# Kernel tuning notes

Hardware: AMD Instinct MI355X
Metric: run time of the kernel (lower is better)

## Reference

```python
import jax, jax.numpy as jnp
import numpy as np

N = 100_000          # nodes
E = 1_600_000        # edges (avg degree 16)
NODE_SCA, NODE_VEC = 4, 3
EDGE_SCA, EDGE_VEC = 6, 3
OUT_SCA, OUT_VEC = 16, 16
CUTOFF = 10.0
EPS = 1e-6
SLOPE_VN = 0.2       # VNLeakyReLU negative slope (SurfGen default)
SLOPE_SCA = 0.01     # nn.LeakyReLU default


def setup_inputs() -> dict:
    key = jax.random.key(0)
    ks = jax.random.split(key, 22)
    rn = lambda k, s: jax.random.normal(k, s, dtype=jnp.float32)
    return {
        # forward args
        'node_sca': rn(ks[0], (N, NODE_SCA)),
        'node_vec': rn(ks[1], (N, NODE_VEC, 3)),
        'edge_sca': rn(ks[2], (E, EDGE_SCA)),
        'edge_vec': rn(ks[3], (E, EDGE_VEC, 3)),
        'gds_dist': jax.random.uniform(ks[4], (E,), dtype=jnp.float32) * 12.0,
        'edge_index': jax.random.randint(ks[5], (2, E), 0, N),
        # message projections (Linear weights stored [in,out])
        'W_nss': rn(ks[6], (NODE_SCA, OUT_SCA)) * 0.3, 'b_nss': rn(ks[7], (OUT_SCA,)) * 0.1,
        'W_ess': rn(ks[8], (EDGE_SCA, OUT_SCA)) * 0.3, 'b_ess': rn(ks[9], (OUT_SCA,)) * 0.1,
        'W_nsv': rn(ks[10], (NODE_SCA, OUT_SCA)) * 0.3, 'b_nsv': rn(ks[11], (OUT_SCA,)) * 0.1,
        'W_esv': rn(ks[12], (EDGE_SCA, OUT_SCA)) * 0.3, 'b_esv': rn(ks[13], (OUT_SCA,)) * 0.1,
        'W_nvv': rn(ks[14], (NODE_VEC, OUT_VEC)) * 0.3,   # VNLinear (no bias)
        'W_evv': rn(ks[15], (EDGE_VEC, OUT_VEC)) * 0.3,
        # GVPerceptronVN(16,16,16,16): GVLinear (dim_hid = 16) + VN LeakyReLU
        'W_lv':  rn(ks[16], (OUT_VEC, OUT_VEC)) * 0.25,   # lin_vector   (no bias)
        'W_lv2': rn(ks[17], (OUT_VEC, OUT_VEC)) * 0.25,   # lin_vector2  (no bias)
        'W_ls':  rn(ks[18], (OUT_VEC + OUT_SCA, OUT_SCA)) * 0.25,  # lin_scalar (no bias)
        'W_gate': rn(ks[19], (OUT_SCA, OUT_VEC)) * 0.25, 'b_gate': rn(ks[20], (OUT_VEC,)) * 0.1,
        'W_dir': rn(ks[21], (OUT_VEC, OUT_VEC)) * 0.25,   # VNLeakyReLU direction (no bias)
    }


def vn_linear(x, W):
    # x: [n, c_in, 3], W: [c_in, c_out] -> [n, c_out, 3]
    return jnp.einsum('nci,co->noi', x, W)


def reference(node_sca, node_vec, edge_sca, edge_vec, gds_dist, edge_index,
              W_nss, b_nss, W_ess, b_ess, W_nsv, b_nsv, W_esv, b_esv,
              W_nvv, W_evv, W_lv, W_lv2, W_ls, W_gate, b_gate, W_dir):
    src = edge_index[0]
    num_nodes = node_sca.shape[0]

    # cosine cutoff coefficient
    coeff = 0.5 * (jnp.cos(gds_dist * (jnp.pi / CUTOFF)) + 1.0)
    coeff = coeff * (gds_dist <= CUTOFF) * (gds_dist >= 0.0)  # [E]

    # scalar message: gather node proj, mix with edge proj, cutoff-weight
    node_ss = node_sca @ W_nss + b_nss                          # [N,16]
    edge_ss = edge_sca @ W_ess + b_ess                          # [E,16]
    msg_sca = node_ss[src] * edge_ss * coeff[:, None]           # [E,16]

    # vector message
    node_vv = vn_linear(node_vec, W_nvv)                        # [N,16,3]
    edge_vv = vn_linear(edge_vec, W_evv)                        # [E,16,3]
    node_sv = node_sca @ W_nsv + b_nsv                          # [N,16]
    edge_sv = edge_sca @ W_esv + b_esv                          # [E,16]
    msg_vec = (node_vv[src] * edge_sv[:, :, None]
               + node_sv[src][:, :, None] * edge_vv) * coeff[:, None, None]  # [E,16,3]

    # scatter_sum into source nodes (matches original's edge_index[0])
    aggr_sca = jax.ops.segment_sum(msg_sca, src, num_segments=num_nodes)  # [N,16]
    aggr_vec = jax.ops.segment_sum(msg_vec, src, num_segments=num_nodes)  # [N,16,3]

    # --- GVPerceptronVN: GVLinear ---
    v_inter = vn_linear(aggr_vec, W_lv)                          # [N,16,3]
    v_norm = jnp.sqrt(jnp.sum(v_inter * v_inter, axis=-1))       # [N,16]
    out_sca = jnp.concatenate([v_norm, aggr_sca], axis=-1) @ W_ls  # [N,16]
    out_vec = vn_linear(v_inter, W_lv2)                          # [N,16,3]
    gate = jax.nn.sigmoid(out_sca @ W_gate + b_gate)[:, :, None]
    out_vec = gate * out_vec

    # --- VNLeakyReLU on vectors ---
    d = vn_linear(out_vec, W_dir)                                # [N,16,3]
    dot = jnp.sum(out_vec * d, axis=-1, keepdims=True)
    mask = (dot >= 0).astype(out_vec.dtype)
    d_norm_sq = jnp.sum(d * d, axis=-1, keepdims=True)
    out_vec = SLOPE_VN * out_vec + (1.0 - SLOPE_VN) * (
        mask * out_vec + (1.0 - mask) * (out_vec - (dot / (d_norm_sq + EPS)) * d))

    # LeakyReLU on scalars
    out_sca = jnp.where(out_sca >= 0, out_sca, SLOPE_SCA * out_sca)
    return out_sca, out_vec
```

## Files before the change

### kernel.cpp

```cpp
#include <hip/hip_runtime.h>
#include <hip/hip_fp16.h>
#include <math.h>

#define CUTOFF_F 10.0f
#define PI_OVER_CUTOFF 0.31415926535897931f
#define KCAP 64
#define KCAP3 32

__global__ __launch_bounds__(256) void bucket_scatter(
    const float* __restrict__ edge_sca,
    const float* __restrict__ edge_vec,
    const float* __restrict__ gds,
    const int* __restrict__ eidx,
    int* __restrict__ count,
    __half* __restrict__ bucket,
    float* __restrict__ aggr,
    int E)
{
    int e = blockIdx.x * blockDim.x + threadIdx.x;
    if (e >= E) return;

    int src = eidx[e];
    float d = gds[e];
    float c = 0.0f;
    if (d >= 0.0f && d <= CUTOFF_F)
        c = 0.5f * (__cosf(d * PI_OVER_CUTOFF) + 1.0f);

    const float* es = edge_sca + (size_t)e * 6;
    const float* ev = edge_vec + (size_t)e * 9;

    float f[16];
#pragma unroll
    for (int i = 0; i < 6; ++i) f[i] = c * es[i];
    f[6] = c;
#pragma unroll
    for (int i = 0; i < 9; ++i) f[7 + i] = c * ev[i];

    int slot = atomicAdd(&count[src], 1);
    if (slot < KCAP3) {
        union { __half h[16]; uint4 u[2]; } pk;
#pragma unroll
        for (int i = 0; i < 16; ++i) pk.h[i] = __float2half(f[i]);
        uint4* pb = (uint4*)(bucket + ((size_t)src * KCAP3 + slot) * 16);
        pb[0] = pk.u[0];
        pb[1] = pk.u[1];
    } else {
        float* base = aggr + (size_t)src * 16;
#pragma unroll
        for (int i = 0; i < 16; ++i) atomicAdd(base + i, f[i]);
    }
}

__global__ __launch_bounds__(256) void count_edges(
    const int* __restrict__ eidx, int* __restrict__ count,
    int* __restrict__ slotOf, int E)
{
    int e = blockIdx.x * blockDim.x + threadIdx.x;
    if (e >= E) return;
    int src = eidx[e];
    slotOf[e] = atomicAdd(&count[src], 1);
}

__global__ __launch_bounds__(256) void scan_block_sums(
    const int* __restrict__ count, int* __restrict__ blockSums, int N)
{
    __shared__ int sdata[256];
    int t = threadIdx.x;
    int i = blockIdx.x * 256 + t;
    sdata[t] = (i < N) ? count[i] : 0;
    __syncthreads();
    for (int off = 128; off > 0; off >>= 1) {
        if (t < off) sdata[t] += sdata[t + off];
        __syncthreads();
    }
    if (t == 0) blockSums[blockIdx.x] = sdata[0];
}

__global__ __launch_bounds__(1024) void scan_exclusive_small(
    int* __restrict__ blockSums, int M)
{
    __shared__ int s[1024];
    int t = threadIdx.x;
    int orig = (t < M) ? blockSums[t] : 0;
    s[t] = orig;
    __syncthreads();
    for (int off = 1; off < 1024; off <<= 1) {
        int v = (t >= off) ? s[t - off] : 0;
        __syncthreads();
        s[t] += v;
        __syncthreads();
    }
    if (t < M) blockSums[t] = s[t] - orig;
}

__global__ __launch_bounds__(256) void scan_final(
    const int* __restrict__ count, const int* __restrict__ blockSums,
    int* __restrict__ offsets, int N)
{
    __shared__ int s[256];
    int t = threadIdx.x;
    int i = blockIdx.x * 256 + t;
    int orig = (i < N) ? count[i] : 0;
    s[t] = orig;
    __syncthreads();
    for (int off = 1; off < 256; off <<= 1) {
        int v = (t >= off) ? s[t - off] : 0;
        __syncthreads();
        s[t] += v;
        __syncthreads();
    }
    if (i < N) offsets[i] = s[t] - orig + blockSums[blockIdx.x];
}

__global__ __launch_bounds__(256) void scatter_payload(
    const float* __restrict__ edge_sca, const float* __restrict__ edge_vec,
    const float* __restrict__ gds, const int* __restrict__ eidx,
    const int* __restrict__ slotOf, const int* __restrict__ offsets,
    __half* __restrict__ payload, int E)
{
    int e = blockIdx.x * blockDim.x + threadIdx.x;
    if (e >= E) return;
    int src = eidx[e];
    float d = gds[e];
    float c = 0.0f;
    if (d >= 0.0f && d <= CUTOFF_F)
        c = 0.5f * (__cosf(d * PI_OVER_CUTOFF) + 1.0f);
    const float* es = edge_sca + (size_t)e * 6;
    const float* ev = edge_vec + (size_t)e * 9;
    union { __half h[16]; uint4 u[2]; } pk;
#pragma unroll
    for (int i = 0; i < 6; ++i) pk.h[i] = __float2half(c * es[i]);
    pk.h[6] = __float2half(c);
#pragma unroll
    for (int i = 0; i < 9; ++i) pk.h[7 + i] = __float2half(c * ev[i]);
    uint4* pb = (uint4*)(payload + (size_t)(offsets[src] + slotOf[e]) * 16);
    pb[0] = pk.u[0];
    pb[1] = pk.u[1];
}

__global__ __launch_bounds__(256) void fill_buckets(
    const int* __restrict__ eidx, int* __restrict__ count,
    int* __restrict__ bucket, int E)
{
    int e = blockIdx.x * blockDim.x + threadIdx.x;
    if (e >= E) return;
    int src = eidx[e];
    int slot = atomicAdd(&count[src], 1);
    if (slot < KCAP) bucket[src * KCAP + slot] = e;
}

__global__ __launch_bounds__(256) void edge_aggregate(
    const float* __restrict__ edge_sca, const float* __restrict__ edge_vec,
    const float* __restrict__ gds, const int* __restrict__ eidx,
    float* __restrict__ aggr, int E)
{
    int e = blockIdx.x * blockDim.x + threadIdx.x;
    if (e >= E) return;
    int src = eidx[e];
    float d = gds[e];
    float coeff = 0.0f;
    if (d >= 0.0f && d <= CUTOFF_F)
        coeff = 0.5f * (__cosf(d * PI_OVER_CUTOFF) + 1.0f);
    float* base = aggr + (size_t)src * 16;
    const float* es = edge_sca + (size_t)e * 6;
    const float* ev = edge_vec + (size_t)e * 9;
#pragma unroll
    for (int c = 0; c < 6; ++c) atomicAdd(base + c, coeff * es[c]);
    atomicAdd(base + 6, coeff);
#pragma unroll
    for (int k = 0; k < 9; ++k) atomicAdd(base + 7 + k, coeff * ev[k]);
}

__global__ __launch_bounds__(256) void node_fused(
    const float* __restrict__ node_sca,
    const float* __restrict__ node_vec,
    const float* __restrict__ edge_sca,
    const float* __restrict__ edge_vec,
    const float* __restrict__ gds,
    const int* __restrict__ count,
    const int* __restrict__ bucket,
    const int* __restrict__ offsets,
    const __half* __restrict__ payload,
    const float* __restrict__ aggr,
    const float* __restrict__ W_nss, const float* __restrict__ b_nss,
    const float* __restrict__ W_ess, const float* __restrict__ b_ess,
    const float* __restrict__ W_nsv, const float* __restrict__ b_nsv,
    const float* __restrict__ W_esv, const float* __restrict__ b_esv,
    const float* __restrict__ W_nvv, const float* __restrict__ W_evv,
    const float* __restrict__ W_lv,  const float* __restrict__ W_lv2,
    const float* __restrict__ W_ls,
    const float* __restrict__ W_gate, const float* __restrict__ b_gate,
    const float* __restrict__ W_dir,
    float* __restrict__ out,
    int N, int mode)
{
    __shared__ float sW_nss[64],  sb_nss[16];
    __shared__ float sW_ess[96],  sb_ess[16];
    __shared__ float sW_nsv[64],  sb_nsv[16];
    __shared__ float sW_esv[96],  sb_esv[16];
    __shared__ float sW_nvv[48],  sW_evv[48];
    __shared__ float sW_lv[256],  sW_lv2[256];
    __shared__ float sW_ls[512];
    __shared__ float sW_gate[256], sb_gate[16];
    __shared__ float sW_dir[256];

    __shared__ float s_in  [16 * 33];
    __shared__ float s_avec[16 * 49];
    __shared__ float s_cat [16 * 33];
    __shared__ float s_vint[16 * 49];
    __shared__ float s_osca[16 * 17];
    __shared__ float s_ovec[16 * 49];

    const int t = threadIdx.x;
    {
        for (int i = t; i < 64;  i += 256) { sW_nss[i] = W_nss[i]; sW_nsv[i] = W_nsv[i]; }
        for (int i = t; i < 96;  i += 256) { sW_ess[i] = W_ess[i]; sW_esv[i] = W_esv[i]; }
        for (int i = t; i < 48;  i += 256) { sW_nvv[i] = W_nvv[i]; sW_evv[i] = W_evv[i]; }
        for (int i = t; i < 256; i += 256) {
            sW_lv[i]   = W_lv[i];
            sW_lv2[i]  = W_lv2[i];
            sW_gate[i] = W_gate[i];
            sW_dir[i]  = W_dir[i];
        }
        for (int i = t; i < 512; i += 256) sW_ls[i] = W_ls[i];
        if (t < 16) {
            sb_nss[t]  = b_nss[t];
            sb_ess[t]  = b_ess[t];
            sb_nsv[t]  = b_nsv[t];
            sb_esv[t]  = b_esv[t];
            sb_gate[t] = b_gate[t];
        }
    }

    const int slot = t >> 4;
    const int o    = t & 15;
    const int n    = blockIdx.x * 16 + slot;
    const bool valid = (n < N);

    if (valid) {
        if (o < 4) s_in[slot * 33 + o]     = node_sca[(size_t)n * 4 + o];
        if (o < 9) s_in[slot * 33 + 4 + o] = node_vec[(size_t)n * 9 + o];
    }

    if (mode == 3) {
        float a0 = 0.f, a1 = 0.f, a2 = 0.f, a3 = 0.f;
        if (valid) {
            int cnt = count[n];
            if (cnt > KCAP3) cnt = KCAP3;
            const __half* p = payload + (size_t)n * KCAP3 * 16 + o;
            int s = 0;
            for (; s + 3 < cnt; s += 4) {
                a0 += __half2float(p[(s + 0) * 16]);
                a1 += __half2float(p[(s + 1) * 16]);
                a2 += __half2float(p[(s + 2) * 16]);
                a3 += __half2float(p[(s + 3) * 16]);
            }
            for (; s < cnt; ++s)
                a0 += __half2float(p[s * 16]);
            a1 += aggr[(size_t)n * 16 + o];
            s_in[slot * 33 + 13 + o] = (a0 + a1) + (a2 + a3);
        }
    } else if (mode == 2) {
        float a0 = 0.f, a1 = 0.f, a2 = 0.f, a3 = 0.f;
        if (valid) {
            int cnt = count[n];
            const __half* p = payload + (size_t)offsets[n] * 16 + o;
            int s = 0;
            for (; s + 3 < cnt; s += 4) {
                a0 += __half2float(p[(size_t)(s + 0) * 16]);
                a1 += __half2float(p[(size_t)(s + 1) * 16]);
                a2 += __half2float(p[(size_t)(s + 2) * 16]);
                a3 += __half2float(p[(size_t)(s + 3) * 16]);
            }
            for (; s < cnt; ++s)
                a0 += __half2float(p[(size_t)s * 16]);
            s_in[slot * 33 + 13 + o] = (a0 + a1) + (a2 + a3);
        }
    } else if (mode == 1) {
        float acc = 0.0f;
        int cnt = valid ? count[n] : 0;
        if (cnt > KCAP) cnt = KCAP;
        const int* bk = bucket + (size_t)n * KCAP;
        for (int s = 0; s < cnt; ++s) {
            int e = bk[s];
            float d = gds[e];
            float coeff = 0.0f;
            if (d >= 0.0f && d <= CUTOFF_F)
                coeff = 0.5f * (__cosf(d * PI_OVER_CUTOFF) + 1.0f);
            float feat;
            if (o < 6)       feat = edge_sca[(size_t)e * 6 + o];
            else if (o == 6) feat = 1.0f;
            else             feat = edge_vec[(size_t)e * 9 + (o - 7)];
            acc += coeff * feat;
        }
        if (valid) s_in[slot * 33 + 13 + o] = acc;
    } else {
        if (valid) s_in[slot * 33 + 13 + o] = aggr[(size_t)n * 16 + o];
    }
    __syncthreads();

    const float* in = s_in + slot * 33;

    float nss = sb_nss[o], nsv = sb_nsv[o];
#pragma unroll
    for (int c = 0; c < 4; ++c) {
        float x = in[c];
        nss += x * sW_nss[c * 16 + o];
        nsv += x * sW_nsv[c * 16 + o];
    }
    float nvv0 = 0.f, nvv1 = 0.f, nvv2 = 0.f;
#pragma unroll
    for (int c = 0; c < 3; ++c) {
        float w = sW_nvv[c * 16 + o];
        nvv0 += in[4 + c * 3 + 0] * w;
        nvv1 += in[4 + c * 3 + 1] * w;
        nvv2 += in[4 + c * 3 + 2] * w;
    }
    float cc = in[19];
    float es = cc * sb_ess[o], ev = cc * sb_esv[o];
#pragma unroll
    for (int c = 0; c < 6; ++c) {
        float a = in[13 + c];
        es += a * sW_ess[c * 16 + o];
        ev += a * sW_esv[c * 16 + o];
    }
    float EV0 = 0.f, EV1 = 0.f, EV2 = 0.f;
#pragma unroll
    for (int c = 0; c < 3; ++c) {
        float w = sW_evv[c * 16 + o];
        EV0 += in[20 + c * 3 + 0] * w;
        EV1 += in[20 + c * 3 + 1] * w;
        EV2 += in[20 + c * 3 + 2] * w;
    }

    float asca = nss * es;
    float av0 = nvv0 * ev + nsv * EV0;
    float av1 = nvv1 * ev + nsv * EV1;
    float av2 = nvv2 * ev + nsv * EV2;
    s_avec[slot * 49 + o * 3 + 0] = av0;
    s_avec[slot * 49 + o * 3 + 1] = av1;
    s_avec[slot * 49 + o * 3 + 2] = av2;
    s_cat[slot * 33 + 16 + o] = asca;
    __syncthreads();

    float vi0 = 0.f, vi1 = 0.f, vi2 = 0.f;
#pragma unroll
    for (int c = 0; c < 16; ++c) {
        float w = sW_lv[c * 16 + o];
        const float* a = &s_avec[slot * 49 + c * 3];
        vi0 += a[0] * w; vi1 += a[1] * w; vi2 += a[2] * w;
    }
    float vnorm = sqrtf(vi0 * vi0 + vi1 * vi1 + vi2 * vi2);
    s_vint[slot * 49 + o * 3 + 0] = vi0;
    s_vint[slot * 49 + o * 3 + 1] = vi1;
    s_vint[slot * 49 + o * 3 + 2] = vi2;
    s_cat[slot * 33 + o] = vnorm;
    __syncthreads();

    float osca = 0.f;
#pragma unroll
    for (int c = 0; c < 32; ++c)
        osca += s_cat[slot * 33 + c] * sW_ls[c * 16 + o];
    float ov0 = 0.f, ov1 = 0.f, ov2 = 0.f;
#pragma unroll
    for (int c = 0; c < 16; ++c) {
        float w = sW_lv2[c * 16 + o];
        const float* a = &s_vint[slot * 49 + c * 3];
        ov0 += a[0] * w; ov1 += a[1] * w; ov2 += a[2] * w;
    }
    s_osca[slot * 17 + o] = osca;
    __syncthreads();

    float g = sb_gate[o];
#pragma unroll
    for (int c = 0; c < 16; ++c)
        g += s_osca[slot * 17 + c] * sW_gate[c * 16 + o];
    g = 1.0f / (1.0f + __expf(-g));
    ov0 *= g; ov1 *= g; ov2 *= g;
    s_ovec[slot * 49 + o * 3 + 0] = ov0;
    s_ovec[slot * 49 + o * 3 + 1] = ov1;
    s_ovec[slot * 49 + o * 3 + 2] = ov2;
    __syncthreads();

    float dv0 = 0.f, dv1 = 0.f, dv2 = 0.f;
#pragma unroll
    for (int c = 0; c < 16; ++c) {
        float w = sW_dir[c * 16 + o];
        const float* a = &s_ovec[slot * 49 + c * 3];
        dv0 += a[0] * w; dv1 += a[1] * w; dv2 += a[2] * w;
    }
    float dot = ov0 * dv0 + ov1 * dv1 + ov2 * dv2;
    if (dot < 0.0f) {
        float dn = dv0 * dv0 + dv1 * dv1 + dv2 * dv2;
        float f = 0.8f * dot / (dn + 1e-6f);
        ov0 -= f * dv0; ov1 -= f * dv1; ov2 -= f * dv2;
    }

    if (valid) {
        float so = (osca >= 0.0f) ? osca : 0.01f * osca;
        out[(size_t)n * 16 + o] = so;
        size_t vb = (size_t)N * 16 + (size_t)n * 48 + (size_t)o * 3;
        out[vb + 0] = ov0;
        out[vb + 1] = ov1;
        out[vb + 2] = ov2;
    }
}

extern "C" void kernel_launch(void* const* d_in, const int* in_sizes, int n_in,
                              void* d_out, int out_size, void* d_ws, size_t ws_size,
                              hipStream_t stream)
{
    const float* node_sca = (const float*)d_in[0];
    const float* node_vec = (const float*)d_in[1];
    const float* edge_sca = (const float*)d_in[2];
    const float* edge_vec = (const float*)d_in[3];
    const float* gds      = (const float*)d_in[4];
    const int*   eidx     = (const int*)d_in[5];

    const int N = in_sizes[0] / 4;
    const int E = in_sizes[4];

    int*    count3  = (int*)d_ws;
    float*  aggr3   = (float*)(count3 + N);
    __half* bucket3 = (__half*)(aggr3 + (size_t)N * 16);
    size_t  need3   = (size_t)N * 4 + (size_t)N * 64
                    + (size_t)N * KCAP3 * 16 * sizeof(__half);

    int*    count     = (int*)d_ws;
    int*    offsets   = count + N;
    int*    blockSums = offsets + N;
    int*    slotOf    = blockSums + 1024;
    size_t  hdr_bytes = ((size_t)(2 * N + 1024 + E) * 4 + 63) & ~(size_t)63;
    __half* payload   = (__half*)((char*)d_ws + hdr_bytes);
    size_t  need_csr  = hdr_bytes + (size_t)E * 16 * sizeof(__half);
    size_t  need_bkt  = (size_t)N * (1 + KCAP) * sizeof(int);

    const int nBlocksN = (N + 255) / 256;

    int mode;
    if (ws_size >= need3)                          mode = 3;
    else if (ws_size >= need_csr && nBlocksN <= 1024) mode = 2;
    else if (ws_size >= need_bkt)                  mode = 1;
    else                                           mode = 0;

    int* bucket = count + N;
    float* aggr = (float*)d_ws;

    if (mode == 3) {
        hipMemsetAsync(count3, 0, (size_t)N * 4 + (size_t)N * 64, stream);
        bucket_scatter<<<(E + 255) / 256, 256, 0, stream>>>(
            edge_sca, edge_vec, gds, eidx, count3, bucket3, aggr3, E);
        node_fused<<<(N + 15) / 16, 256, 0, stream>>>(
            node_sca, node_vec, edge_sca, edge_vec, gds,
            count3, bucket, offsets, bucket3, aggr3,
            (const float*)d_in[6],  (const float*)d_in[7],
            (const float*)d_in[8],  (const float*)d_in[9],
            (const float*)d_in[10], (const float*)d_in[11],
            (const float*)d_in[12], (const float*)d_in[13],
            (const float*)d_in[14], (const float*)d_in[15],
            (const float*)d_in[16], (const float*)d_in[17],
            (const float*)d_in[18],
            (const float*)d_in[19], (const float*)d_in[20],
            (const float*)d_in[21],
            (float*)d_out, N, 3);
        return;
    }

    if (mode == 2) {
        hipMemsetAsync(count, 0, (size_t)N * sizeof(int), stream);
        count_edges<<<(E + 255) / 256, 256, 0, stream>>>(eidx, count, slotOf, E);
        scan_block_sums<<<nBlocksN, 256, 0, stream>>>(count, blockSums, N);
        scan_exclusive_small<<<1, 1024, 0, stream>>>(blockSums, nBlocksN);
        scan_final<<<nBlocksN, 256, 0, stream>>>(count, blockSums, offsets, N);
        scatter_payload<<<(E + 255) / 256, 256, 0, stream>>>(
            edge_sca, edge_vec, gds, eidx, slotOf, offsets, payload, E);
    } else if (mode == 1) {
        hipMemsetAsync(count, 0, (size_t)N * sizeof(int), stream);
        fill_buckets<<<(E + 255) / 256, 256, 0, stream>>>(eidx, count, bucket, E);
    } else {
        hipMemsetAsync(aggr, 0, (size_t)N * 16 * sizeof(float), stream);
        edge_aggregate<<<(E + 255) / 256, 256, 0, stream>>>(
            edge_sca, edge_vec, gds, eidx, aggr, E);
    }

    node_fused<<<(N + 15) / 16, 256, 0, stream>>>(
        node_sca, node_vec, edge_sca, edge_vec, gds,
        count, bucket, offsets, payload, aggr,
        (const float*)d_in[6],  (const float*)d_in[7],
        (const float*)d_in[8],  (const float*)d_in[9],
        (const float*)d_in[10], (const float*)d_in[11],
        (const float*)d_in[12], (const float*)d_in[13],
        (const float*)d_in[14], (const float*)d_in[15],
        (const float*)d_in[16], (const float*)d_in[17],
        (const float*)d_in[18],
        (const float*)d_in[19], (const float*)d_in[20],
        (const float*)d_in[21],
        (float*)d_out, N, mode);
}
```

Measured before the change: 305.7 us.

## Use slot-major bucket layout and process four edges per thread in scatter

The per-node edge bucket changes from node-major [N][KCAP3][16] to slot-major [KCAP3][N][16], and the reader in node_fused is updated to the new stride. Consecutive nodes in a block now read contiguous 32-byte chunks for the same slot instead of 1 KB-strided regions. The scatter kernel also handles four edges per thread with a grid-stride pattern, which cuts the block count and gives each thread more independent memory operations in flight. Scatter writes are random in either layout, and reading higher slots now touches widely separated memory pages.

Result: slower. 317.7 us (+3.9%).

```diff
diff --git a/kernel.cpp b/kernel.cpp
--- a/kernel.cpp
+++ b/kernel.cpp
@@ -15,39 +15,45 @@
     int* __restrict__ count,
     __half* __restrict__ bucket,
     float* __restrict__ aggr,
-    int E)
-{
-    int e = blockIdx.x * blockDim.x + threadIdx.x;
-    if (e >= E) return;
-
-    int src = eidx[e];
-    float d = gds[e];
-    float c = 0.0f;
-    if (d >= 0.0f && d <= CUTOFF_F)
-        c = 0.5f * (__cosf(d * PI_OVER_CUTOFF) + 1.0f);
-
-    const float* es = edge_sca + (size_t)e * 6;
-    const float* ev = edge_vec + (size_t)e * 9;
-
-    float f[16];
-#pragma unroll
-    for (int i = 0; i < 6; ++i) f[i] = c * es[i];
-    f[6] = c;
-#pragma unroll
-    for (int i = 0; i < 9; ++i) f[7 + i] = c * ev[i];
-
-    int slot = atomicAdd(&count[src], 1);
-    if (slot < KCAP3) {
-        union { __half h[16]; uint4 u[2]; } pk;
-#pragma unroll
-        for (int i = 0; i < 16; ++i) pk.h[i] = __float2half(f[i]);
-        uint4* pb = (uint4*)(bucket + ((size_t)src * KCAP3 + slot) * 16);
-        pb[0] = pk.u[0];
-        pb[1] = pk.u[1];
-    } else {
-        float* base = aggr + (size_t)src * 16;
-#pragma unroll
-        for (int i = 0; i < 16; ++i) atomicAdd(base + i, f[i]);
+    int E, int N)
+{
+    const int tid = blockIdx.x * blockDim.x + threadIdx.x;
+    const int T   = gridDim.x * blockDim.x;
+
+#pragma unroll
+    for (int k = 0; k < 4; ++k) {
+        int e = tid + k * T;
+        if (e >= E) continue;
+
+        int src = eidx[e];
+        float d = gds[e];
+        float c = 0.0f;
+        if (d >= 0.0f && d <= CUTOFF_F)
+            c = 0.5f * (__cosf(d * PI_OVER_CUTOFF) + 1.0f);
+
+        const float* es = edge_sca + (size_t)e * 6;
+        const float* ev = edge_vec + (size_t)e * 9;
+
+        float f[16];
+#pragma unroll
+        for (int i = 0; i < 6; ++i) f[i] = c * es[i];
+        f[6] = c;
+#pragma unroll
+        for (int i = 0; i < 9; ++i) f[7 + i] = c * ev[i];
+
+        int slot = atomicAdd(&count[src], 1);
+        if (slot < KCAP3) {
+            union { __half h[16]; uint4 u[2]; } pk;
+#pragma unroll
+            for (int i = 0; i < 16; ++i) pk.h[i] = __float2half(f[i]);
+            uint4* pb = (uint4*)(bucket + ((size_t)slot * N + src) * 16);
+            pb[0] = pk.u[0];
+            pb[1] = pk.u[1];
+        } else {
+            float* base = aggr + (size_t)src * 16;
+#pragma unroll
+            for (int i = 0; i < 16; ++i) atomicAdd(base + i, f[i]);
+        }
     }
 }
 
@@ -247,16 +253,17 @@
         if (valid) {
             int cnt = count[n];
             if (cnt > KCAP3) cnt = KCAP3;
-            const __half* p = payload + (size_t)n * KCAP3 * 16 + o;
+            const __half* p = payload + (size_t)n * 16 + o;
+            const size_t stride = (size_t)N * 16;
             int s = 0;
             for (; s + 3 < cnt; s += 4) {
-                a0 += __half2float(p[(s + 0) * 16]);
-                a1 += __half2float(p[(s + 1) * 16]);
-                a2 += __half2float(p[(s + 2) * 16]);
-                a3 += __half2float(p[(s + 3) * 16]);
+                a0 += __half2float(p[(size_t)(s + 0) * stride]);
+                a1 += __half2float(p[(size_t)(s + 1) * stride]);
+                a2 += __half2float(p[(size_t)(s + 2) * stride]);
+                a3 += __half2float(p[(size_t)(s + 3) * stride]);
             }
             for (; s < cnt; ++s)
-                a0 += __half2float(p[s * 16]);
+                a0 += __half2float(p[(size_t)s * stride]);
             a1 += aggr[(size_t)n * 16 + o];
             s_in[slot * 33 + 13 + o] = (a0 + a1) + (a2 + a3);
         }
@@ -438,18 +445,19 @@
     const int nBlocksN = (N + 255) / 256;
 
     int mode;
-    if (ws_size >= need3)                          mode = 3;
+    if (ws_size >= need3)                             mode = 3;
     else if (ws_size >= need_csr && nBlocksN <= 1024) mode = 2;
-    else if (ws_size >= need_bkt)                  mode = 1;
-    else                                           mode = 0;
+    else if (ws_size >= need_bkt)                     mode = 1;
+    else                                              mode = 0;
 
     int* bucket = count + N;
     float* aggr = (float*)d_ws;
 
     if (mode == 3) {
         hipMemsetAsync(count3, 0, (size_t)N * 4 + (size_t)N * 64, stream);
-        bucket_scatter<<<(E + 255) / 256, 256, 0, stream>>>(
-            edge_sca, edge_vec, gds, eidx, count3, bucket3, aggr3, E);
+        int nB = (E + 4 * 256 - 1) / (4 * 256);
+        bucket_scatter<<<nB, 256, 0, stream>>>(
+            edge_sca, edge_vec, gds, eidx, count3, bucket3, aggr3, E, N);
         node_fused<<<(N + 15) / 16, 256, 0, stream>>>(
             node_sca, node_vec, edge_sca, edge_vec, gds,
             count3, bucket, offsets, bucket3, aggr3,
```
